# Kernel optimization log

Measured on AMD Instinct MI355X. Metric: run time of the kernel, lower is better.

## Reference

```python
import jax, jax.numpy as jnp
import numpy as np

B, N, T, F_IN, F_OUT = 4, 2048, 12, 32, 32
ALPHA = 0.2  # leaky relu negative slope
NEG_INF = -9e15


def setup_inputs() -> dict:
    key = jax.random.key(0)
    k = jax.random.split(key, 6)
    x = jax.random.normal(k[0], (B, N, T, F_IN), dtype=jnp.float32)
    adj = jax.random.randint(k[1], (N, N), 0, 2, dtype=jnp.int32)
    W = jax.random.normal(k[2], (T * F_IN, T * F_OUT), dtype=jnp.float32) * 0.05
    a = jax.random.normal(k[3], (2 * T * F_OUT, 1), dtype=jnp.float32) * 0.05
    conv_w = jax.random.normal(k[4], (T, T, 3), dtype=jnp.float32) * 0.1  # (out_ch, in_ch, k)
    conv_b = jnp.zeros((T,), dtype=jnp.float32)
    return {"x": x, "adj": adj, "W": W, "a": a, "conv_w": conv_w, "conv_b": conv_b}


def reference(x, adj, W, a, conv_w, conv_b):
    Bz, Nn, Tt, Fi = x.shape
    Fo = W.shape[1] // Tt
    # temporal conv: channels = timesteps, length = nodes*features
    xt = x.transpose(0, 2, 1, 3).reshape(Bz, Tt, Nn * Fi)  # (B,T,L)
    xt = jax.lax.conv_general_dilated(
        xt, conv_w, window_strides=(1,), padding=[(1, 1)],
        dimension_numbers=("NCH", "OIH", "NCH")) + conv_b[None, :, None]
    xt = xt.reshape(Bz, Tt, Nn, Fi).transpose(0, 2, 1, 3).reshape(Bz, Nn, Tt * Fi)
    Wh = xt @ W  # (B, N, T*Fo)
    # e[b,i,j] = leakyrelu(Wh[b,i].a1 + Wh[b,j].a2)  -- avoids O(N^2 * 2F) concat
    a1 = a[: Tt * Fo, 0]
    a2 = a[Tt * Fo:, 0]
    f1 = Wh @ a1  # (B, N)
    f2 = Wh @ a2  # (B, N)
    e = jax.nn.leaky_relu(f1[:, :, None] + f2[:, None, :], negative_slope=ALPHA)
    e = jnp.where(adj[None, :, :] > 0, e, NEG_INF)
    attn = jax.nn.softmax(e, axis=-1)  # (B, N, N); dropout omitted (eval mode)
    h_prime = attn @ Wh  # (B, N, T*Fo)
    return jax.nn.elu(h_prime).reshape(Bz, Nn, Tt, Fo)
```

## Files before the change

### kernel.cpp

```cpp
#include <hip/hip_runtime.h>

using short8 = __attribute__((ext_vector_type(8))) short;
using f32x4  = __attribute__((ext_vector_type(4))) float;
using f32x16 = __attribute__((ext_vector_type(16))) float;

__device__ __forceinline__ unsigned short f2bf(float f) {
  unsigned u = __float_as_uint(f);
  u += 0x7fffu + ((u >> 16) & 1u);
  return (unsigned short)(u >> 16);
}

__global__ __launch_bounds__(256) void transpose_f2b_kernel(const float* __restrict__ in,
                                                            unsigned short* __restrict__ out,
                                                            int rows, int cols) {
  __shared__ float tile[32][33];
  const int r0 = blockIdx.x * 32, c0 = blockIdx.y * 32;
  const int li = threadIdx.x >> 5, ci = threadIdx.x & 31;
#pragma unroll
  for (int p = 0; p < 4; ++p) {
    int r = li + p * 8;
    tile[r][ci] = in[(size_t)(r0 + r) * cols + c0 + ci];
  }
  __syncthreads();
#pragma unroll
  for (int p = 0; p < 4; ++p) {
    int c = li + p * 8;
    out[(size_t)(c0 + c) * rows + r0 + ci] = f2bf(tile[ci][c]);
  }
}

__global__ __launch_bounds__(256) void adjmask_kernel(const int* __restrict__ adj,
                                                      unsigned* __restrict__ adjm) {
  const int wv = (blockIdx.x << 2) + (threadIdx.x >> 6);
  const int lane = threadIdx.x & 63;
  const int row = wv >> 5, j0 = (wv & 31) << 6;
  unsigned long long mask = __ballot(adj[(size_t)row * 2048 + j0 + lane] > 0);
  if (lane == 0) {
    adjm[row * 64 + (j0 >> 5)]     = (unsigned)mask;
    adjm[row * 64 + (j0 >> 5) + 1] = (unsigned)(mask >> 32);
  }
}

__global__ __launch_bounds__(256) void gemm_wh4_kernel(const float* __restrict__ x,
                                                       const float* __restrict__ cw,
                                                       const float* __restrict__ cb,
                                                       const unsigned short* __restrict__ Wt,
                                                       const float* __restrict__ a,
                                                       unsigned short* __restrict__ whp,
                                                       float* __restrict__ f1,
                                                       float* __restrict__ f2) {
  __shared__ __align__(16) char lds[24768 + 12544 + 1792 + 128];
  float* xin = (float*)lds;
  unsigned short* atile = (unsigned short*)lds;
  unsigned short* wtile = (unsigned short*)(lds + 24768);
  float* cws = (float*)(lds + 24768 + 12544);
  float* cbs = cws + 432;
  float* s1s = (float*)(lds + 24768 + 12544 + 1792);
  float* s2s = s1s + 16;

  const int tid = threadIdx.x;
  const int rb = blockIdx.x;
  const int b = rb >> 7, jg2 = rb & 127;
  const int r0 = rb << 4;
  const int w = tid >> 6, lane = tid & 63;
  const int il = lane & 15, kg = lane >> 4;

  for (int i = tid; i < 432; i += 256) cws[i] = cw[i];
  if (tid < 12) cbs[tid] = cb[tid];
  if (tid < 16) { s1s[tid] = 0.f; s2s[tid] = 0.f; }
  const float* xb = x + (size_t)b * 2048 * 12 * 32;
#pragma unroll
  for (int t = 0; t < 12; ++t) {
    for (int i = tid; i < 514; i += 256) {
      const int gp = jg2 * 512 + i - 1;
      float v = 0.f;
      if ((unsigned)gp < 65536u) v = xb[((size_t)(gp >> 5) * 12 + t) * 32 + (gp & 31)];
      xin[t * 516 + i] = v;
    }
  }
  __syncthreads();

  const int ploc = tid * 2;
  float accv0[12], accv1[12];
#pragma unroll
  for (int to = 0; to < 12; ++to) { accv0[to] = cbs[to]; accv1[to] = cbs[to]; }
#pragma unroll
  for (int ti = 0; ti < 12; ++ti) {
    const float x0 = xin[ti * 516 + ploc];
    const float x1 = xin[ti * 516 + ploc + 1];
    const float x2 = xin[ti * 516 + ploc + 2];
    const float x3 = xin[ti * 516 + ploc + 3];
#pragma unroll
    for (int to = 0; to < 12; ++to) {
      const float* wp = &cws[(to * 12 + ti) * 3];
      const float w0 = wp[0], w1 = wp[1], w2 = wp[2];
      accv0[to] += x0 * w0 + x1 * w1 + x2 * w2;
      accv1[to] += x1 * w0 + x2 * w1 + x3 * w2;
    }
  }
  __syncthreads();

  {
    const int row = ploc >> 5, f = ploc & 31;
    unsigned* ap32 = (unsigned*)(atile + row * 392 + f);
#pragma unroll
    for (int to = 0; to < 12; ++to) {
      const unsigned lo = f2bf(accv0[to]), hi = f2bf(accv1[to]);
      ap32[to * 16] = lo | (hi << 16);
    }
  }
  __syncthreads();

  f32x4 acc[6];
#pragma unroll
  for (int t = 0; t < 6; ++t) acc[t] = (f32x4){0.f, 0.f, 0.f, 0.f};
  const unsigned short* arow = atile + il * 392 + kg * 8;
#pragma unroll
  for (int kk = 0; kk < 12; ++kk) {
    short8 af = *reinterpret_cast<const short8*>(arow + kk * 32);
#pragma unroll
    for (int t = 0; t < 6; ++t) {
      const int c = w * 96 + t * 16 + il;
      short8 bf = *reinterpret_cast<const short8*>(Wt + (size_t)c * 384 + kk * 32 + kg * 8);
      acc[t] = __builtin_amdgcn_mfma_f32_16x16x32_bf16(af, bf, acc[t], 0, 0, 0);
    }
  }
  float p1[4] = {0.f, 0.f, 0.f, 0.f}, p2[4] = {0.f, 0.f, 0.f, 0.f};
#pragma unroll
  for (int t = 0; t < 6; ++t) {
    const int c = w * 96 + t * 16 + il;
    const float a1v = a[c], a2v = a[384 + c];
#pragma unroll
    for (int r = 0; r < 4; ++r) { p1[r] += acc[t][r] * a1v; p2[r] += acc[t][r] * a2v; }
  }
#pragma unroll
  for (int off = 1; off < 16; off <<= 1) {
#pragma unroll
    for (int r = 0; r < 4; ++r) { p1[r] += __shfl_xor(p1[r], off); p2[r] += __shfl_xor(p2[r], off); }
  }
  if (il == 0) {
#pragma unroll
    for (int r = 0; r < 4; ++r) {
      atomicAdd(&s1s[kg * 4 + r], p1[r]);
      atomicAdd(&s2s[kg * 4 + r], p2[r]);
    }
  }
#pragma unroll
  for (int t = 0; t < 6; ++t)
#pragma unroll
    for (int r = 0; r < 4; ++r)
      wtile[(kg * 4 + r) * 392 + w * 96 + t * 16 + il] = f2bf(acc[t][r]);
  __syncthreads();

#pragma unroll
  for (int rep = 0; rep < 3; ++rep) {
    const int flat = rep * 256 + tid;
    const int ct32 = flat >> 6, l = flat & 63;
    const int l5 = l & 31, hw2 = l >> 5;
    short8 v;
#pragma unroll
    for (int e = 0; e < 8; ++e)
      v[e] = (short)wtile[(hw2 * 8 + e) * 392 + ct32 * 32 + l5];
    *reinterpret_cast<short8*>((char*)whp +
        ((((size_t)b * 128 + jg2) * 12 + ct32) << 10) + l * 16) = v;
  }
  if (tid < 16) { f1[r0 + tid] = s1s[tid]; f2[r0 + tid] = s2s[tid]; }
}

__global__ __launch_bounds__(256) void f2max_kernel(const float* __restrict__ f2,
                                                    float* __restrict__ gmax) {
  __shared__ float wm[4];
  const int b = blockIdx.x;
  const int tid = threadIdx.x;
  float m = -3.0e38f;
  for (int i = tid; i < 2048; i += 256) m = fmaxf(m, f2[b * 2048 + i]);
#pragma unroll
  for (int off = 32; off; off >>= 1) m = fmaxf(m, __shfl_xor(m, off));
  if ((tid & 63) == 0) wm[tid >> 6] = m;
  __syncthreads();
  if (tid == 0) gmax[b] = fmaxf(fmaxf(wm[0], wm[1]), fmaxf(wm[2], wm[3]));
}

__global__ __launch_bounds__(256, 3) void attn13_kernel(const float* __restrict__ f1,
                                                        const float* __restrict__ f2,
                                                        const unsigned* __restrict__ adjm,
                                                        const unsigned short* __restrict__ whp,
                                                        const float* __restrict__ gmax,
                                                        float* __restrict__ out) {
  __shared__ float red[4][32][64];
  __shared__ float dred[128];
  const int bi = blockIdx.x;
  const int combo = bi % 12;
  const int b  = combo & 3;
  const int ch = combo >> 2;
  const int i0 = (bi / 12) << 5;
  const int tid = threadIdx.x;
  const int ks = tid >> 6;
  const int lane = tid & 63;
  const int l5 = lane & 31, hw = lane >> 5;
  const int hw8 = hw * 8;
  const int ig = i0 + l5;

  const unsigned* adjr = adjm + (size_t)ig * 64 + ks * 16;
  const float* f2b = f2 + b * 2048 + ks * 512 + hw8;
  const char* pbase = (const char*)whp +
      ((((size_t)b * 128 + ks * 32) * 12 + ch * 4) << 10) + lane * 16;

  const float f1v = f1[b * 2048 + ig];
  const float gm = gmax[b];
  const float mz = f1v + gm;
  const float m  = fmaxf(mz, 0.2f * mz);
  const float Az = f1v - m;
  const float Bz = 0.2f * f1v - m;

  const f32x16 zero16 = {0.f,0.f,0.f,0.f,0.f,0.f,0.f,0.f,0.f,0.f,0.f,0.f,0.f,0.f,0.f,0.f};
  f32x16 acc[4];
#pragma unroll
  for (int t = 0; t < 4; ++t) acc[t] = zero16;
  float denom = 0.f;

  short8 bA[4], bB[4];
  float4 fA0, fA1, fB0, fB1;
  unsigned wC, wN;

#define LOADB(AR, KK)                                                                   \
  { _Pragma("unroll")                                                                   \
    for (int tt = 0; tt < 4; ++tt)                                                      \
      AR[tt] = *reinterpret_cast<const short8*>(pbase + (size_t)(KK) * 12288 +          \
                                                (size_t)tt * 1024); }

#define PEL(GV, BIT, DST)                                                               \
  { const float z_ = Az + (GV);                                                         \
    const float e_ = fmaxf(z_, fmaf((GV), 0.2f, Bz));                                   \
    DST = ((bits_ >> (BIT)) & 1u) ? __expf(e_) : 0.f; }

#define PKBF(HI, LO) (((__float_as_uint(HI) + 0x8000u) & 0xffff0000u) |                 \
                      ((__float_as_uint(LO) + 0x8000u) >> 16))

#define STEPD(AR, F0, F1, SH, KK, DL)                                                   \
  { const unsigned bits_ = wC >> ((SH) + hw8);                                          \
    float p0_, p1_, p2_, p3_, p4_, p5_, p6_, p7_;                                       \
    PEL(F0.x, 0, p0_)  PEL(F0.y, 1, p1_)  PEL(F0.z, 2, p2_)  PEL(F0.w, 3, p3_)          \
    PEL(F1.x, 4, p4_)  PEL(F1.y, 5, p5_)  PEL(F1.z, 6, p6_)  PEL(F1.w, 7, p7_)          \
    denom += (((p0_ + p1_) + (p2_ + p3_)) + ((p4_ + p5_) + (p6_ + p7_)));               \
    union { unsigned u[4]; short8 s8; } cc;                                             \
    cc.u[0] = PKBF(p1_, p0_); cc.u[1] = PKBF(p3_, p2_);                                 \
    cc.u[2] = PKBF(p5_, p4_); cc.u[3] = PKBF(p7_, p6_);                                 \
    _Pragma("unroll")                                                                   \
    for (int tt = 0; tt < 4; ++tt)                                                      \
      acc[tt] = __builtin_amdgcn_mfma_f32_32x32x16_bf16(cc.s8, AR[tt], acc[tt], 0, 0, 0); \
    if (DL) {                                                                           \
      LOADB(AR, (KK) + 2)                                                               \
      const float* fp_ = f2b + ((KK) + 2) * 16;                                         \
      F0 = *reinterpret_cast<const float4*>(fp_);                                       \
      F1 = *reinterpret_cast<const float4*>(fp_ + 4);                                   \
    } }

  LOADB(bA, 0) LOADB(bB, 1)
  fA0 = *reinterpret_cast<const float4*>(f2b);
  fA1 = *reinterpret_cast<const float4*>(f2b + 4);
  fB0 = *reinterpret_cast<const float4*>(f2b + 16);
  fB1 = *reinterpret_cast<const float4*>(f2b + 20);
  wC = adjr[0];
  wN = adjr[1];

  for (int t = 0; t < 16; ++t) {
    STEPD(bA, fA0, fA1, 0, 2 * t, (t < 15))
    STEPD(bB, fB0, fB1, 16, 2 * t + 1, (t < 15))
    wC = wN;
    wN = adjr[(t + 2 < 16) ? t + 2 : 15];
  }
#undef LOADB
#undef PEL
#undef PKBF
#undef STEPD

  float dn = denom + __shfl_xor(denom, 32);
  if (hw == 0) dred[ks * 32 + l5] = dn;

#pragma unroll
  for (int r = 0; r < 2; ++r) {
#pragma unroll
    for (int tt = 0; tt < 2; ++tt) {
#pragma unroll
      for (int q = 0; q < 16; ++q) {
        const int row = (q & 3) + 8 * (q >> 2) + 4 * hw;
        red[ks][row][tt * 32 + l5] = acc[r * 2 + tt][q];
      }
    }
    __syncthreads();
    const size_t ob = ((size_t)b * 2048 + i0) * 384 + ch * 128 + r * 64;
#pragma unroll
    for (int p = 0; p < 8; ++p) {
      const int idx = p * 256 + tid;
      const int row = idx >> 6;
      const int c = idx & 63;
      float v = red[0][row][c] + red[1][row][c] + red[2][row][c] + red[3][row][c];
      const float d = dred[row] + dred[32 + row] + dred[64 + row] + dred[96 + row];
      v /= d;
      v = v > 0.f ? v : expm1f(v);
      out[ob + (size_t)row * 384 + c] = v;
    }
    __syncthreads();
  }
}

extern "C" void kernel_launch(void* const* d_in, const int* in_sizes, int n_in,
                              void* d_out, int out_size, void* d_ws, size_t ws_size,
                              hipStream_t stream) {
  const float* x  = (const float*)d_in[0];
  const int* adj  = (const int*)d_in[1];
  const float* W  = (const float*)d_in[2];
  const float* a  = (const float*)d_in[3];
  const float* cw = (const float*)d_in[4];
  const float* cb = (const float*)d_in[5];
  float* out = (float*)d_out;

  char* ws = (char*)d_ws;
  unsigned short* Wt  = (unsigned short*)ws; ws += (size_t)147456 * 2;
  unsigned short* whp = (unsigned short*)ws; ws += (size_t)3145728 * 2;
  float* f1           = (float*)ws;          ws += (size_t)8192 * 4;
  float* f2           = (float*)ws;          ws += (size_t)8192 * 4;
  unsigned* adjm      = (unsigned*)ws;       ws += (size_t)2048 * 64 * 4;
  float* gmax         = (float*)ws;          ws += 64;

  transpose_f2b_kernel<<<dim3(12, 12), 256, 0, stream>>>(W, Wt, 384, 384);
  adjmask_kernel<<<dim3(16384), 256, 0, stream>>>(adj, adjm);
  gemm_wh4_kernel<<<dim3(512), 256, 0, stream>>>(x, cw, cb, Wt, a, whp, f1, f2);
  f2max_kernel<<<dim3(4), 256, 0, stream>>>(f2, gmax);
  attn13_kernel<<<dim3(768), 256, 0, stream>>>(f1, f2, adjm, whp, gmax, out);
}
```

Measured before the change: 88.06 us.

## Split Wh GEMM columns across two blocks with pre-packed W fragments

```diff
diff --git a/kernel.cpp b/kernel.cpp
--- a/kernel.cpp
+++ b/kernel.cpp
@@ -10,27 +10,23 @@
   return (unsigned short)(u >> 16);
 }
 
-__global__ __launch_bounds__(256) void transpose_f2b_kernel(const float* __restrict__ in,
-                                                            unsigned short* __restrict__ out,
-                                                            int rows, int cols) {
-  __shared__ float tile[32][33];
-  const int r0 = blockIdx.x * 32, c0 = blockIdx.y * 32;
-  const int li = threadIdx.x >> 5, ci = threadIdx.x & 31;
-#pragma unroll
-  for (int p = 0; p < 4; ++p) {
-    int r = li + p * 8;
-    tile[r][ci] = in[(size_t)(r0 + r) * cols + c0 + ci];
-  }
-  __syncthreads();
-#pragma unroll
-  for (int p = 0; p < 4; ++p) {
-    int c = li + p * 8;
-    out[(size_t)(c0 + c) * rows + r0 + ci] = f2bf(tile[ci][c]);
-  }
+__global__ __launch_bounds__(256) void pack_w_kernel(const float* __restrict__ W,
+                                                     unsigned short* __restrict__ wtp) {
+  const int f = blockIdx.x * 4 + (threadIdx.x >> 6);
+  const int l = threadIdx.x & 63;
+  const int kk = f / 24, ct = f % 24;
+  const int il = l & 15, kg = l >> 4;
+  const float* src = W + (size_t)(kk * 32 + kg * 8) * 384 + ct * 16 + il;
+  short8 v;
+#pragma unroll
+  for (int e = 0; e < 8; ++e) v[e] = (short)f2bf(src[(size_t)e * 384]);
+  *reinterpret_cast<short8*>((char*)wtp + ((size_t)f << 10) + l * 16) = v;
 }
 
 __global__ __launch_bounds__(256) void adjmask_kernel(const int* __restrict__ adj,
-                                                      unsigned* __restrict__ adjm) {
+                                                      unsigned* __restrict__ adjm,
+                                                      float* __restrict__ f12) {
+  if (blockIdx.x < 64) f12[blockIdx.x * 256 + threadIdx.x] = 0.f;
   const int wv = (blockIdx.x << 2) + (threadIdx.x >> 6);
   const int lane = threadIdx.x & 63;
   const int row = wv >> 5, j0 = (wv & 31) << 6;
@@ -41,33 +37,32 @@
   }
 }
 
-__global__ __launch_bounds__(256) void gemm_wh4_kernel(const float* __restrict__ x,
+__global__ __launch_bounds__(256) void gemm_wh5_kernel(const float* __restrict__ x,
                                                        const float* __restrict__ cw,
                                                        const float* __restrict__ cb,
-                                                       const unsigned short* __restrict__ Wt,
+                                                       const unsigned short* __restrict__ wtp,
                                                        const float* __restrict__ a,
                                                        unsigned short* __restrict__ whp,
                                                        float* __restrict__ f1,
                                                        float* __restrict__ f2) {
-  __shared__ __align__(16) char lds[24768 + 12544 + 1792 + 128];
+  __shared__ __align__(16) char lds[24768 + 6400 + 1792];
   float* xin = (float*)lds;
   unsigned short* atile = (unsigned short*)lds;
   unsigned short* wtile = (unsigned short*)(lds + 24768);
-  float* cws = (float*)(lds + 24768 + 12544);
+  float* cws = (float*)(lds + 24768 + 6400);
   float* cbs = cws + 432;
-  float* s1s = (float*)(lds + 24768 + 12544 + 1792);
-  float* s2s = s1s + 16;
 
   const int tid = threadIdx.x;
   const int rb = blockIdx.x;
-  const int b = rb >> 7, jg2 = rb & 127;
-  const int r0 = rb << 4;
+  const int b = rb >> 8;
+  const int jg2 = (rb >> 1) & 127;
+  const int ch2 = rb & 1;
+  const int r0 = ((b << 7) + jg2) << 4;
   const int w = tid >> 6, lane = tid & 63;
   const int il = lane & 15, kg = lane >> 4;
 
   for (int i = tid; i < 432; i += 256) cws[i] = cw[i];
   if (tid < 12) cbs[tid] = cb[tid];
-  if (tid < 16) { s1s[tid] = 0.f; s2s[tid] = 0.f; }
   const float* xb = x + (size_t)b * 2048 * 12 * 32;
 #pragma unroll
   for (int t = 0; t < 12; ++t) {
@@ -111,24 +106,36 @@
   }
   __syncthreads();
 
-  f32x4 acc[6];
-#pragma unroll
-  for (int t = 0; t < 6; ++t) acc[t] = (f32x4){0.f, 0.f, 0.f, 0.f};
+  f32x4 acc[3];
+#pragma unroll
+  for (int t = 0; t < 3; ++t) acc[t] = (f32x4){0.f, 0.f, 0.f, 0.f};
   const unsigned short* arow = atile + il * 392 + kg * 8;
+  const int ct0 = ch2 * 12 + w * 3;
+  const char* wb = (const char*)wtp + ((size_t)ct0 << 10) + lane * 16;
+
+  short8 bcur[3], bnxt[3];
+#pragma unroll
+  for (int t = 0; t < 3; ++t)
+    bcur[t] = *reinterpret_cast<const short8*>(wb + ((size_t)t << 10));
 #pragma unroll
   for (int kk = 0; kk < 12; ++kk) {
+    if (kk < 11) {
+#pragma unroll
+      for (int t = 0; t < 3; ++t)
+        bnxt[t] = *reinterpret_cast<const short8*>(wb + (((size_t)(kk + 1) * 24 + t) << 10));
+    }
     short8 af = *reinterpret_cast<const short8*>(arow + kk * 32);
 #pragma unroll
-    for (int t = 0; t < 6; ++t) {
-      const int c = w * 96 + t * 16 + il;
-      short8 bf = *reinterpret_cast<const short8*>(Wt + (size_t)c * 384 + kk * 32 + kg * 8);
-      acc[t] = __builtin_amdgcn_mfma_f32_16x16x32_bf16(af, bf, acc[t], 0, 0, 0);
-    }
-  }
+    for (int t = 0; t < 3; ++t)
+      acc[t] = __builtin_amdgcn_mfma_f32_16x16x32_bf16(af, bcur[t], acc[t], 0, 0, 0);
+#pragma unroll
+    for (int t = 0; t < 3; ++t) bcur[t] = bnxt[t];
+  }
+
   float p1[4] = {0.f, 0.f, 0.f, 0.f}, p2[4] = {0.f, 0.f, 0.f, 0.f};
 #pragma unroll
-  for (int t = 0; t < 6; ++t) {
-    const int c = w * 96 + t * 16 + il;
+  for (int t = 0; t < 3; ++t) {
+    const int c = (ct0 + t) * 16 + il;
     const float a1v = a[c], a2v = a[384 + c];
 #pragma unroll
     for (int r = 0; r < 4; ++r) { p1[r] += acc[t][r] * a1v; p2[r] += acc[t][r] * a2v; }
@@ -141,30 +148,32 @@
   if (il == 0) {
 #pragma unroll
     for (int r = 0; r < 4; ++r) {
-      atomicAdd(&s1s[kg * 4 + r], p1[r]);
-      atomicAdd(&s2s[kg * 4 + r], p2[r]);
-    }
-  }
-#pragma unroll
-  for (int t = 0; t < 6; ++t)
+      atomicAdd(&f1[r0 + kg * 4 + r], p1[r]);
+      atomicAdd(&f2[r0 + kg * 4 + r], p2[r]);
+    }
+  }
+#pragma unroll
+  for (int t = 0; t < 3; ++t)
 #pragma unroll
     for (int r = 0; r < 4; ++r)
-      wtile[(kg * 4 + r) * 392 + w * 96 + t * 16 + il] = f2bf(acc[t][r]);
-  __syncthreads();
-
-#pragma unroll
-  for (int rep = 0; rep < 3; ++rep) {
+      wtile[(kg * 4 + r) * 200 + (w * 3 + t) * 16 + il] = f2bf(acc[t][r]);
+  __syncthreads();
+
+#pragma unroll
+  for (int rep = 0; rep < 2; ++rep) {
     const int flat = rep * 256 + tid;
-    const int ct32 = flat >> 6, l = flat & 63;
-    const int l5 = l & 31, hw2 = l >> 5;
-    short8 v;
-#pragma unroll
-    for (int e = 0; e < 8; ++e)
-      v[e] = (short)wtile[(hw2 * 8 + e) * 392 + ct32 * 32 + l5];
-    *reinterpret_cast<short8*>((char*)whp +
-        ((((size_t)b * 128 + jg2) * 12 + ct32) << 10) + l * 16) = v;
-  }
-  if (tid < 16) { f1[r0 + tid] = s1s[tid]; f2[r0 + tid] = s2s[tid]; }
+    if (flat < 384) {
+      const int ct32l = flat >> 6, l = flat & 63;
+      const int l5 = l & 31, hw2 = l >> 5;
+      short8 v;
+#pragma unroll
+      for (int e = 0; e < 8; ++e)
+        v[e] = (short)wtile[(hw2 * 8 + e) * 200 + ct32l * 32 + l5];
+      const int ct32g = ch2 * 6 + ct32l;
+      *reinterpret_cast<short8*>((char*)whp +
+          ((((size_t)b * 128 + jg2) * 12 + ct32g) << 10) + l * 16) = v;
+    }
+  }
 }
 
 __global__ __launch_bounds__(256) void f2max_kernel(const float* __restrict__ f2,
@@ -317,16 +326,16 @@
   float* out = (float*)d_out;
 
   char* ws = (char*)d_ws;
-  unsigned short* Wt  = (unsigned short*)ws; ws += (size_t)147456 * 2;
+  unsigned short* wtp = (unsigned short*)ws; ws += (size_t)147456 * 2;
   unsigned short* whp = (unsigned short*)ws; ws += (size_t)3145728 * 2;
   float* f1           = (float*)ws;          ws += (size_t)8192 * 4;
   float* f2           = (float*)ws;          ws += (size_t)8192 * 4;
   unsigned* adjm      = (unsigned*)ws;       ws += (size_t)2048 * 64 * 4;
   float* gmax         = (float*)ws;          ws += 64;
 
-  transpose_f2b_kernel<<<dim3(12, 12), 256, 0, stream>>>(W, Wt, 384, 384);
-  adjmask_kernel<<<dim3(16384), 256, 0, stream>>>(adj, adjm);
-  gemm_wh4_kernel<<<dim3(512), 256, 0, stream>>>(x, cw, cb, Wt, a, whp, f1, f2);
+  pack_w_kernel<<<dim3(72), 256, 0, stream>>>(W, wtp);
+  adjmask_kernel<<<dim3(16384), 256, 0, stream>>>(adj, adjm, f1);
+  gemm_wh5_kernel<<<dim3(1024), 256, 0, stream>>>(x, cw, cb, wtp, a, whp, f1, f2);
   f2max_kernel<<<dim3(4), 256, 0, stream>>>(f2, gmax);
   attn13_kernel<<<dim3(768), 256, 0, stream>>>(f1, f2, adjm, whp, gmax, out);
 }
```

After: 79.79 us. 9.4% less time.
